# Kernel tuning notes

Measured on AMD Instinct MI355X. Metric: run time of the kernel, lower is better.

The kernel has to match this reference:

```python
import jax, jax.numpy as jnp
import numpy as np

FL = 48  # featurelength


def _sage(x, src, dst, Wl, bl, Wr):
    # PyG SAGEConv (mean aggr): lin_l(mean_{j in N(i)} x_j) + lin_r(x_i); bias on lin_l.
    N = x.shape[0]
    agg = jax.ops.segment_sum(x[src], dst, num_segments=N)
    cnt = jax.ops.segment_sum(jnp.ones((src.shape[0], 1), x.dtype), dst, num_segments=N)
    mean = agg / jnp.maximum(cnt, 1.0)
    return mean @ Wl + bl + x @ Wr


def _pool2(x, H):
    # x: (H*H, C) node features on an HxH grid -> 2x2 max pool -> (H/2*H/2, C)
    C = x.shape[1]
    xc = x.T.reshape(C, H // 2, 2, H // 2, 2)
    return xc.max(axis=(2, 4)).reshape(C, (H // 2) * (H // 2)).T


def _att_block(x, src, dst, am_W, am_b, ax_W, ax_b, c_Wl, c_bl, c_Wr):
    # spatial attention: sigmoid(fc(mean) + fc(max)) over nodes, per-channel gate
    att = jax.nn.sigmoid(jnp.mean(x, 0)[None] @ am_W + am_b + jnp.max(x, 0)[None] @ ax_W + ax_b)
    # channel attention: SAGEConv -> (N,1) gate broadcast over channels
    ch = jax.nn.sigmoid(_sage(x, src, dst, c_Wl, c_bl, c_Wr))
    return x + x * att + x * ch


def setup_inputs() -> dict:
    key = jax.random.key(0)
    ks = iter(jax.random.split(key, 64))
    d = {}
    d['x_image'] = jax.random.normal(next(ks), (128, 128), jnp.float32)
    sizes = [(16384, 65536), (4096, 16384), (1024, 4096), (256, 1024)]
    for i, (n, e) in enumerate(sizes):
        d[f'e{i}'] = jax.random.randint(next(ks), (2, e), 0, n)
    d['train'] = 0

    def lin(kin, kout, k):
        s = 1.0 / np.sqrt(kin)
        return jax.random.uniform(k, (kin, kout), jnp.float32, -s, s)

    # gconv1..4 (in: 1,48,48,48 -> out 48)
    for i, cin in enumerate([1, FL, FL, FL], start=1):
        d[f'g{i}_Wl'] = lin(cin, FL, next(ks))
        d[f'g{i}_bl'] = jnp.zeros((FL,), jnp.float32)
        d[f'g{i}_Wr'] = lin(cin, FL, next(ks))
    # attention blocks 1..4
    for i in range(1, 5):
        d[f'am{i}_W'] = lin(FL, FL, next(ks)); d[f'am{i}_b'] = jnp.zeros((FL,), jnp.float32)
        d[f'ax{i}_W'] = lin(FL, FL, next(ks)); d[f'ax{i}_b'] = jnp.zeros((FL,), jnp.float32)
        d[f'c{i}_Wl'] = lin(FL, 1, next(ks)); d[f'c{i}_bl'] = jnp.zeros((1,), jnp.float32)
        d[f'c{i}_Wr'] = lin(FL, 1, next(ks))
    d['fc1_W'] = lin(FL * 16 * 16, 256, next(ks)); d['fc1_b'] = jnp.zeros((256,), jnp.float32)
    d['fc2_W'] = lin(256, 10, next(ks)); d['fc2_b'] = jnp.zeros((10,), jnp.float32)
    return d


def reference(x_image,
              g1_Wl, g1_bl, g1_Wr, g2_Wl, g2_bl, g2_Wr,
              g3_Wl, g3_bl, g3_Wr, g4_Wl, g4_bl, g4_Wr,
              am1_W, am1_b, ax1_W, ax1_b, c1_Wl, c1_bl, c1_Wr,
              am2_W, am2_b, ax2_W, ax2_b, c2_Wl, c2_bl, c2_Wr,
              am3_W, am3_b, ax3_W, ax3_b, c3_Wl, c3_bl, c3_Wr,
              am4_W, am4_b, ax4_W, ax4_b, c4_Wl, c4_bl, c4_Wr,
              fc1_W, fc1_b, fc2_W, fc2_b,
              e0, e1, e2, e3, train):
    x = x_image.reshape(128 * 128, 1)  # (16384, 1) node features
    # level 1: SAGE on 128x128 graph, pool to 64x64, attention on 64x64 graph (e1)
    x = jax.nn.relu(_sage(x, e0[0], e0[1], g1_Wl, g1_bl, g1_Wr))
    x = _pool2(x, 128)
    x = _att_block(x, e1[0], e1[1], am1_W, am1_b, ax1_W, ax1_b, c1_Wl, c1_bl, c1_Wr)
    # level 2
    x = jax.nn.relu(_sage(x, e1[0], e1[1], g2_Wl, g2_bl, g2_Wr))
    x = _pool2(x, 64)
    x = _att_block(x, e2[0], e2[1], am2_W, am2_b, ax2_W, ax2_b, c2_Wl, c2_bl, c2_Wr)
    # level 3
    x = jax.nn.relu(_sage(x, e2[0], e2[1], g3_Wl, g3_bl, g3_Wr))
    x = _pool2(x, 32)
    x = _att_block(x, e3[0], e3[1], am3_W, am3_b, ax3_W, ax3_b, c3_Wl, c3_bl, c3_Wr)
    # level 4 (no pool; flatten channels-major like torch transpose+reshape)
    x = jax.nn.relu(_sage(x, e3[0], e3[1], g4_Wl, g4_bl, g4_Wr))  # (256, 48)
    x = x.T.reshape(1, FL * 16 * 16)
    x = jax.nn.relu(x @ fc1_W + fc1_b)
    logits = x @ fc2_W + fc2_b
    return jax.nn.log_softmax(logits, axis=1)
```

## Files before the change

### kernel.cpp

```cpp
#include <hip/hip_runtime.h>
#include <math.h>

#define FL 48

__device__ __forceinline__ float sigmoidf(float v) { return 1.0f / (1.0f + expf(-v)); }

__device__ __forceinline__ void att_lds(const float* sum, const float* mxv, float invN,
                                        const float* amW, const float* amb,
                                        const float* axW, const float* axb, float* sAtt) {
  int t = threadIdx.x;
  if (t < FL) {
    float s = amb[t] + axb[t];
    for (int ci = 0; ci < FL; ++ci)
      s += (sum[ci] * invN) * amW[ci * FL + t] + mxv[ci] * axW[ci * FL + t];
    sAtt[t] = sigmoidf(s);
  }
}


__global__ __launch_bounds__(256) void k_prep(
    const int* __restrict__ e0, const int* __restrict__ e1,
    const int* __restrict__ e2, const int* __restrict__ e3,
    const float* __restrict__ ximg,
    float* __restrict__ cnt0, float* __restrict__ cnt1,
    float* __restrict__ cnt2, float* __restrict__ cnt3,
    float* __restrict__ aggS0) {
  int g = blockIdx.x * 256 + threadIdx.x;
  if (g < 65536) {
    int d = e0[65536 + g];
    atomicAdd(&cnt0[d], 1.0f);
    atomicAdd(&aggS0[d], ximg[e0[g]]);
  } else if (g < 81920) {
    atomicAdd(&cnt1[e1[16384 + (g - 65536)]], 1.0f);
  } else if (g < 86016) {
    atomicAdd(&cnt2[e2[4096 + (g - 81920)]], 1.0f);
  } else if (g < 87040) {
    atomicAdd(&cnt3[e3[1024 + (g - 86016)]], 1.0f);
  }
}

__global__ __launch_bounds__(256) void k_scan(
    const float* __restrict__ cnt1, int* __restrict__ off1,
    const float* __restrict__ cnt2, int* __restrict__ off2,
    const float* __restrict__ cnt3, int* __restrict__ off3) {
  const float* cnt; int* off; int N;
  if (blockIdx.x == 0) { cnt = cnt1; off = off1; N = 4096; }
  else if (blockIdx.x == 1) { cnt = cnt2; off = off2; N = 1024; }
  else { cnt = cnt3; off = off3; N = 256; }
  __shared__ int part[256];
  int t = threadIdx.x;
  int chunk = N / 256;
  int base = t * chunk;
  int s = 0;
  for (int i = 0; i < chunk; ++i) s += (int)cnt[base + i];
  part[t] = s;
  __syncthreads();
  for (int o = 1; o < 256; o <<= 1) {
    int v = (t >= o) ? part[t - o] : 0;
    __syncthreads();
    part[t] += v;
    __syncthreads();
  }
  int run = part[t] - s;
  for (int i = 0; i < chunk; ++i) { off[base + i] = run; run += (int)cnt[base + i]; }
  if (t == 255) off[N] = part[255];
}

__global__ __launch_bounds__(256) void k_fill_s1(
    const int* __restrict__ e1, const int* __restrict__ e2, const int* __restrict__ e3,
    const int* __restrict__ off1, int* __restrict__ cur1, int* __restrict__ csr1,
    const int* __restrict__ off2, int* __restrict__ cur2, int* __restrict__ csr2,
    const int* __restrict__ off3, int* __restrict__ cur3, int* __restrict__ csr3,
    const float* __restrict__ ximg, const float* __restrict__ aggS0,
    const float* __restrict__ cnt0,
    const float* __restrict__ Wl, const float* __restrict__ bl, const float* __restrict__ Wr,
    float* __restrict__ xp1) {
  int blk = blockIdx.x;
  if (blk < 84) {
    int i = blk * 256 + threadIdx.x;
    if (i < 16384) {
      int s = e1[i], d = e1[16384 + i];
      csr1[off1[d] + atomicAdd(&cur1[d], 1)] = s;
    } else if (i < 20480) {
      int ii = i - 16384;
      int s = e2[ii], d = e2[4096 + ii];
      csr2[off2[d] + atomicAdd(&cur2[d], 1)] = s;
    } else if (i < 21504) {
      int ii = i - 20480;
      int s = e3[ii], d = e3[1024 + ii];
      csr3[off3[d] + atomicAdd(&cur3[d], 1)] = s;
    }
  } else {
    int g = (blk - 84) * 256 + threadIdx.x;
    if (g < 4096 * FL) {
      int c = g % FL, m = g / FL;
      int a = m >> 6, b = m & 63;
      float wl = Wl[c], wr = Wr[c], bb = bl[c];
      float best = -INFINITY;
#pragma unroll
      for (int da = 0; da < 2; ++da)
#pragma unroll
        for (int db = 0; db < 2; ++db) {
          int n = (2 * a + da) * 128 + (2 * b + db);
          float mean = aggS0[n] / fmaxf(cnt0[n], 1.0f);
          best = fmaxf(best, fmaxf(mean * wl + bb + ximg[n] * wr, 0.0f));
        }
      xp1[g] = best;
    }
  }
}

__global__ __launch_bounds__(256) void k_A(
    const float* __restrict__ x, int N,
    const int* __restrict__ csr, const int* __restrict__ off,
    const float* __restrict__ cntf,
    const float* __restrict__ cWl, const float* __restrict__ cWr,
    const float* __restrict__ cbl,
    float* __restrict__ sum, float* __restrict__ mxv, float* __restrict__ ch) {
  if (blockIdx.x < FL) {
    int c = blockIdx.x, t = threadIdx.x;
    float s = 0.0f, m = -INFINITY;
    for (int n = t; n < N; n += 256) {
      float v = x[n * FL + c];
      s += v; m = fmaxf(m, v);
    }
    __shared__ float ss[256], sm[256];
    ss[t] = s; sm[t] = m;
    __syncthreads();
    for (int o = 128; o > 0; o >>= 1) {
      if (t < o) { ss[t] += ss[t + o]; sm[t] = fmaxf(sm[t], sm[t + o]); }
      __syncthreads();
    }
    if (t == 0) { sum[c] = ss[0]; mxv[c] = sm[0]; }
  } else {
    int n = (blockIdx.x - FL) * 256 + threadIdx.x;
    if (n >= N) return;
    const float* xr = x + n * FL;
    float dr = 0.0f;
    for (int c = 0; c < FL; ++c) dr += xr[c] * cWr[c];
    float g = 0.0f;
    int j0 = off[n], j1 = off[n + 1];
    for (int j = j0; j < j1; ++j) {
      const float* xs = x + csr[j] * FL;
      float a = 0.0f;
      for (int c = 0; c < FL; ++c) a += xs[c] * cWl[c];
      g += a;
    }
    float mean = g / fmaxf(cntf[n], 1.0f);
    ch[n] = sigmoidf(mean + cbl[0] + dr);
  }
}

template <int POOL>
__global__ __launch_bounds__(256) void k_B(
    const float* __restrict__ x, int N, int H,
    const int* __restrict__ csr, const int* __restrict__ off,
    const float* __restrict__ cntf, const float* __restrict__ ch,
    const float* __restrict__ sum, const float* __restrict__ mxv,
    const float* __restrict__ amW, const float* __restrict__ amb,
    const float* __restrict__ axW, const float* __restrict__ axb,
    const float* __restrict__ Wl, const float* __restrict__ bl,
    const float* __restrict__ Wr,
    float* __restrict__ y) {
  const int NS = POOL ? 16 : 4;
  __shared__ float sWl[FL * FL], sWr[FL * FL], sAtt[FL];
  __shared__ float smean[16][FL], sx[16][FL];
  int t = threadIdx.x;
  att_lds(sum, mxv, 1.0f / (float)N, amW, amb, axW, axb, sAtt);
  for (int i = t; i < FL * FL; i += 256) { sWl[i] = Wl[i]; sWr[i] = Wr[i]; }
  __syncthreads();
  int Ho = H >> 1;
  for (int idx = t; idx < NS * FL; idx += 256) {
    int k = idx / FL, ci = idx % FL;
    int m = blockIdx.x * 4 + (POOL ? (k >> 2) : k);
    int n;
    if (POOL) {
      int a = m / Ho, b = m % Ho;
      n = (2 * a + ((k >> 1) & 1)) * H + (2 * b + (k & 1));
    } else {
      n = m;
    }
    float g1 = 1.0f + sAtt[ci];
    float acc = 0.0f;
    for (int j = off[n]; j < off[n + 1]; ++j) {
      int s = csr[j];
      acc += x[s * FL + ci] * (g1 + ch[s]);
    }
    smean[k][ci] = acc / fmaxf(cntf[n], 1.0f);
    sx[k][ci] = x[n * FL + ci] * (g1 + ch[n]);
  }
  __syncthreads();
  if (t < 4 * FL) {
    int q = t / FL, c = t % FL;
    int m = blockIdx.x * 4 + q;
    float best = -INFINITY;
#pragma unroll
    for (int sub = 0; sub < (POOL ? 4 : 1); ++sub) {
      int k = POOL ? q * 4 + sub : q;
      float s = bl[c];
      for (int ci = 0; ci < FL; ++ci)
        s += smean[k][ci] * sWl[ci * FL + c] + sx[k][ci] * sWr[ci * FL + c];
      best = fmaxf(best, fmaxf(s, 0.0f));
    }
    y[m * FL + c] = best;
  }
}

__global__ __launch_bounds__(256) void k_fc1(const float* __restrict__ x4,
                                             const float* __restrict__ W,
                                             float* __restrict__ acc) {
  __shared__ float xin[96];
  int k0 = blockIdx.x * 96;
  int t = threadIdx.x;
  if (t < 96) {
    int k = k0 + t;
    xin[t] = x4[(k & 255) * FL + (k >> 8)];
  }
  __syncthreads();
  float a = 0.0f;
  for (int i = 0; i < 96; ++i) a += xin[i] * W[(size_t)(k0 + i) * 256 + t];
  atomicAdd(&acc[t], a);
}

__global__ void k_final(const float* __restrict__ acc, const float* __restrict__ b1,
                        const float* __restrict__ W2, const float* __restrict__ b2,
                        float* __restrict__ out) {
  __shared__ float av[256];
  __shared__ float logits[10];
  int t = threadIdx.x;
  av[t] = fmaxf(acc[t] + b1[t], 0.0f);
  __syncthreads();
  if (t < 10) {
    float s = b2[t];
    for (int o = 0; o < 256; ++o) s += av[o] * W2[o * 10 + t];
    logits[t] = s;
  }
  __syncthreads();
  if (t == 0) {
    float m = logits[0];
    for (int j = 1; j < 10; ++j) m = fmaxf(m, logits[j]);
    float s = 0.0f;
    for (int j = 0; j < 10; ++j) s += expf(logits[j] - m);
    float ls = logf(s);
    for (int j = 0; j < 10; ++j) out[j] = logits[j] - m - ls;
  }
}


static inline int cdiv(int a, int b) { return (a + b - 1) / b; }

extern "C" void kernel_launch(void* const* d_in, const int* in_sizes, int n_in,
                              void* d_out, int out_size, void* d_ws, size_t ws_size,
                              hipStream_t stream) {
  const float* ximg = (const float*)d_in[0];
  const int* e0 = (const int*)d_in[1];
  const int* e1 = (const int*)d_in[2];
  const int* e2 = (const int*)d_in[3];
  const int* e3 = (const int*)d_in[4];
  const float* g1Wl = (const float*)d_in[6];
  const float* g1bl = (const float*)d_in[7];
  const float* g1Wr = (const float*)d_in[8];
  const float* gWl[3] = {(const float*)d_in[9], (const float*)d_in[12], (const float*)d_in[15]};
  const float* gbl[3] = {(const float*)d_in[10], (const float*)d_in[13], (const float*)d_in[16]};
  const float* gWr[3] = {(const float*)d_in[11], (const float*)d_in[14], (const float*)d_in[17]};
  const float* amW[3]; const float* amb[3]; const float* axW[3]; const float* axb[3];
  const float* cWl[3]; const float* cbl[3]; const float* cWr[3];
  for (int i = 0; i < 3; ++i) {
    int base = 18 + i * 7;
    amW[i] = (const float*)d_in[base + 0];
    amb[i] = (const float*)d_in[base + 1];
    axW[i] = (const float*)d_in[base + 2];
    axb[i] = (const float*)d_in[base + 3];
    cWl[i] = (const float*)d_in[base + 4];
    cbl[i] = (const float*)d_in[base + 5];
    cWr[i] = (const float*)d_in[base + 6];
  }
  const float* fc1W = (const float*)d_in[46];
  const float* fc1b = (const float*)d_in[47];
  const float* fc2W = (const float*)d_in[48];
  const float* fc2b = (const float*)d_in[49];
  float* out = (float*)d_out;

  const int N0 = 16384, N1 = 4096, N2 = 1024, N3 = 256;
  const int E1 = 16384, E2 = 4096, E3 = 1024;

  char* basep = (char*)d_ws;
  size_t off = 0;
  auto alloc = [&](size_t bytes) -> void* {
    void* q = basep + off;
    off += (bytes + 4095) & ~(size_t)4095;
    return q;
  };
  float* cnt0 = (float*)alloc(N0 * 4);
  float* cnt1 = (float*)alloc(N1 * 4);
  float* cnt2 = (float*)alloc(N2 * 4);
  float* cnt3 = (float*)alloc(N3 * 4);
  float* aggS0 = (float*)alloc(N0 * 4);
  int* cur1 = (int*)alloc(N1 * 4);
  int* cur2 = (int*)alloc(N2 * 4);
  int* cur3 = (int*)alloc(N3 * 4);
  float* fc1acc = (float*)alloc(256 * 4);
  size_t zbytes = off;
  int* off1 = (int*)alloc((N1 + 1) * 4);
  int* off2 = (int*)alloc((N2 + 1) * 4);
  int* off3 = (int*)alloc((N3 + 1) * 4);
  int* csr1 = (int*)alloc(E1 * 4);
  int* csr2 = (int*)alloc(E2 * 4);
  int* csr3 = (int*)alloc(E3 * 4);
  float* sum1 = (float*)alloc(FL * 4); float* max1 = (float*)alloc(FL * 4);
  float* sum2 = (float*)alloc(FL * 4); float* max2 = (float*)alloc(FL * 4);
  float* sum3 = (float*)alloc(FL * 4); float* max3 = (float*)alloc(FL * 4);
  float* ch2 = (float*)alloc(N1 * 4);
  float* ch3 = (float*)alloc(N2 * 4);
  float* ch4 = (float*)alloc(N3 * 4);
  float* xp1 = (float*)alloc(N1 * FL * 4);
  float* xp2 = (float*)alloc(N2 * FL * 4);
  float* xp3 = (float*)alloc(N3 * FL * 4);
  float* x4 = (float*)alloc(N3 * FL * 4);

  hipMemsetAsync(d_ws, 0, zbytes, stream);
  k_prep<<<cdiv(87040, 256), 256, 0, stream>>>(e0, e1, e2, e3, ximg,
                                               cnt0, cnt1, cnt2, cnt3, aggS0);
  k_scan<<<3, 256, 0, stream>>>(cnt1, off1, cnt2, off2, cnt3, off3);
  k_fill_s1<<<84 + cdiv(N1 * FL, 256), 256, 0, stream>>>(
      e1, e2, e3, off1, cur1, csr1, off2, cur2, csr2, off3, cur3, csr3,
      ximg, aggS0, cnt0, g1Wl, g1bl, g1Wr, xp1);

  k_A<<<FL + cdiv(N1, 256), 256, 0, stream>>>(xp1, N1, csr1, off1, cnt1,
                                              cWl[0], cWr[0], cbl[0], sum1, max1, ch2);
  k_B<1><<<N2 / 4, 256, 0, stream>>>(xp1, N1, 64, csr1, off1, cnt1, ch2, sum1, max1,
                                     amW[0], amb[0], axW[0], axb[0],
                                     gWl[0], gbl[0], gWr[0], xp2);
  k_A<<<FL + cdiv(N2, 256), 256, 0, stream>>>(xp2, N2, csr2, off2, cnt2,
                                              cWl[1], cWr[1], cbl[1], sum2, max2, ch3);
  k_B<1><<<N3 / 4, 256, 0, stream>>>(xp2, N2, 32, csr2, off2, cnt2, ch3, sum2, max2,
                                     amW[1], amb[1], axW[1], axb[1],
                                     gWl[1], gbl[1], gWr[1], xp3);
  k_A<<<FL + cdiv(N3, 256), 256, 0, stream>>>(xp3, N3, csr3, off3, cnt3,
                                              cWl[2], cWr[2], cbl[2], sum3, max3, ch4);
  k_B<0><<<N3 / 4, 256, 0, stream>>>(xp3, N3, 16, csr3, off3, cnt3, ch4, sum3, max3,
                                     amW[2], amb[2], axW[2], axb[2],
                                     gWl[2], gbl[2], gWr[2], x4);

  k_fc1<<<128, 256, 0, stream>>>(x4, fc1W, fc1acc);
  k_final<<<1, 256, 0, stream>>>(fc1acc, fc1b, fc2W, fc2b, out);

  (void)in_sizes; (void)n_in; (void)out_size; (void)ws_size;
}
```

Baseline: 108.7 us.

## Fuse graph build and attention stats into producer kernels, cut launch count

Builds each CSR (count, scan, fill) inside a single block in shared memory, which replaces the separate prep, scan and fill kernels. The per-node channel-gate dot products and the per-channel sum and max are folded into the epilogue of the producing kernel (k_s1 or k_B), so the k_A launches go away. Consumers rebuild the sigmoid gate from neighbour sums of the dot products. Launches drop from about ten to six, at the cost of redundant neighbour gate computation, atomic float max done through unsigned bit patterns (valid only while values are non-negative, as after ReLU), and padded accumulators to spread atomic contention.

Result: slower. 156.0 us (+43.6%).

```diff
diff --git a/kernel.cpp b/kernel.cpp
--- a/kernel.cpp
+++ b/kernel.cpp
@@ -2,57 +2,50 @@
 #include <math.h>
 
 #define FL 48
+#define STP 16
 
 __device__ __forceinline__ float sigmoidf(float v) { return 1.0f / (1.0f + expf(-v)); }
 
-__device__ __forceinline__ void att_lds(const float* sum, const float* mxv, float invN,
-                                        const float* amW, const float* amb,
-                                        const float* axW, const float* axb, float* sAtt) {
-  int t = threadIdx.x;
-  if (t < FL) {
-    float s = amb[t] + axb[t];
-    for (int ci = 0; ci < FL; ++ci)
-      s += (sum[ci] * invN) * amW[ci * FL + t] + mxv[ci] * axW[ci * FL + t];
-    sAtt[t] = sigmoidf(s);
-  }
-}
-
-
-__global__ __launch_bounds__(256) void k_prep(
-    const int* __restrict__ e0, const int* __restrict__ e1,
-    const int* __restrict__ e2, const int* __restrict__ e3,
-    const float* __restrict__ ximg,
-    float* __restrict__ cnt0, float* __restrict__ cnt1,
-    float* __restrict__ cnt2, float* __restrict__ cnt3,
-    float* __restrict__ aggS0) {
-  int g = blockIdx.x * 256 + threadIdx.x;
-  if (g < 65536) {
-    int d = e0[65536 + g];
+__device__ __forceinline__ float ch_node(int s, const int* __restrict__ csr,
+                                         const int* __restrict__ off,
+                                         const float* __restrict__ dl,
+                                         const float* __restrict__ dr, float cb) {
+  int j0 = off[s], j1 = off[s + 1];
+  float g = 0.0f;
+  for (int j = j0; j < j1; ++j) g += dl[csr[j]];
+  return sigmoidf(g / fmaxf((float)(j1 - j0), 1.0f) + cb + dr[s]);
+}
+
+
+__global__ __launch_bounds__(256) void k_graph(
+    const int* __restrict__ e0, const float* __restrict__ ximg,
+    float* __restrict__ cnt0, float* __restrict__ aggS0,
+    const int* __restrict__ e1, int* __restrict__ off1, int* __restrict__ csr1,
+    const int* __restrict__ e2, int* __restrict__ off2, int* __restrict__ csr2,
+    const int* __restrict__ e3, int* __restrict__ off3, int* __restrict__ csr3) {
+  int blk = blockIdx.x;
+  if (blk < 256) {
+    int i = blk * 256 + threadIdx.x;
+    int d = e0[65536 + i];
     atomicAdd(&cnt0[d], 1.0f);
-    atomicAdd(&aggS0[d], ximg[e0[g]]);
-  } else if (g < 81920) {
-    atomicAdd(&cnt1[e1[16384 + (g - 65536)]], 1.0f);
-  } else if (g < 86016) {
-    atomicAdd(&cnt2[e2[4096 + (g - 81920)]], 1.0f);
-  } else if (g < 87040) {
-    atomicAdd(&cnt3[e3[1024 + (g - 86016)]], 1.0f);
-  }
-}
-
-__global__ __launch_bounds__(256) void k_scan(
-    const float* __restrict__ cnt1, int* __restrict__ off1,
-    const float* __restrict__ cnt2, int* __restrict__ off2,
-    const float* __restrict__ cnt3, int* __restrict__ off3) {
-  const float* cnt; int* off; int N;
-  if (blockIdx.x == 0) { cnt = cnt1; off = off1; N = 4096; }
-  else if (blockIdx.x == 1) { cnt = cnt2; off = off2; N = 1024; }
-  else { cnt = cnt3; off = off3; N = 256; }
+    atomicAdd(&aggS0[d], ximg[e0[i]]);
+    return;
+  }
+  __shared__ int buf[4096];
   __shared__ int part[256];
-  int t = threadIdx.x;
+  const int* e; int* off; int* csr; int N, E;
+  if (blk == 256)      { e = e1; off = off1; csr = csr1; N = 4096; E = 16384; }
+  else if (blk == 257) { e = e2; off = off2; csr = csr2; N = 1024; E = 4096; }
+  else                 { e = e3; off = off3; csr = csr3; N = 256;  E = 1024; }
+  int t = threadIdx.x;
+  for (int n = t; n < N; n += 256) buf[n] = 0;
+  __syncthreads();
+  for (int i = t; i < E; i += 256) atomicAdd(&buf[e[E + i]], 1);
+  __syncthreads();
   int chunk = N / 256;
   int base = t * chunk;
   int s = 0;
-  for (int i = 0; i < chunk; ++i) s += (int)cnt[base + i];
+  for (int i = 0; i < chunk; ++i) s += buf[base + i];
   part[t] = s;
   __syncthreads();
   for (int o = 1; o < 256; o <<= 1) {
@@ -62,134 +55,139 @@
     __syncthreads();
   }
   int run = part[t] - s;
-  for (int i = 0; i < chunk; ++i) { off[base + i] = run; run += (int)cnt[base + i]; }
-  if (t == 255) off[N] = part[255];
-}
-
-__global__ __launch_bounds__(256) void k_fill_s1(
-    const int* __restrict__ e1, const int* __restrict__ e2, const int* __restrict__ e3,
-    const int* __restrict__ off1, int* __restrict__ cur1, int* __restrict__ csr1,
-    const int* __restrict__ off2, int* __restrict__ cur2, int* __restrict__ csr2,
-    const int* __restrict__ off3, int* __restrict__ cur3, int* __restrict__ csr3,
+  for (int i = 0; i < chunk; ++i) {
+    int c = buf[base + i];
+    off[base + i] = run;
+    buf[base + i] = run;
+    run += c;
+  }
+  if (t == 255) off[N] = E;
+  __syncthreads();
+  for (int i = t; i < E; i += 256) {
+    int d = e[E + i];
+    int pos = atomicAdd(&buf[d], 1);
+    csr[pos] = e[i];
+  }
+}
+
+__global__ __launch_bounds__(256) void k_s1(
     const float* __restrict__ ximg, const float* __restrict__ aggS0,
     const float* __restrict__ cnt0,
-    const float* __restrict__ Wl, const float* __restrict__ bl, const float* __restrict__ Wr,
-    float* __restrict__ xp1) {
-  int blk = blockIdx.x;
-  if (blk < 84) {
-    int i = blk * 256 + threadIdx.x;
-    if (i < 16384) {
-      int s = e1[i], d = e1[16384 + i];
-      csr1[off1[d] + atomicAdd(&cur1[d], 1)] = s;
-    } else if (i < 20480) {
-      int ii = i - 16384;
-      int s = e2[ii], d = e2[4096 + ii];
-      csr2[off2[d] + atomicAdd(&cur2[d], 1)] = s;
-    } else if (i < 21504) {
-      int ii = i - 20480;
-      int s = e3[ii], d = e3[1024 + ii];
-      csr3[off3[d] + atomicAdd(&cur3[d], 1)] = s;
-    }
-  } else {
-    int g = (blk - 84) * 256 + threadIdx.x;
-    if (g < 4096 * FL) {
-      int c = g % FL, m = g / FL;
-      int a = m >> 6, b = m & 63;
-      float wl = Wl[c], wr = Wr[c], bb = bl[c];
-      float best = -INFINITY;
+    const float* __restrict__ Wl, const float* __restrict__ bl,
+    const float* __restrict__ Wr,
+    const float* __restrict__ cWl, const float* __restrict__ cWr,
+    float* __restrict__ y, float* __restrict__ dl, float* __restrict__ dr,
+    float* __restrict__ sumP, float* __restrict__ maxP) {
+  __shared__ float ldl[4], ldr[4], lsum[FL];
+  __shared__ unsigned lmax[FL];
+  int t = threadIdx.x;
+  if (t < 4) { ldl[t] = 0.0f; ldr[t] = 0.0f; }
+  if (t < FL) { lsum[t] = 0.0f; lmax[t] = 0u; }
+  __syncthreads();
+  if (t < 4 * FL) {
+    int q = t / FL, c = t % FL;
+    int m = blockIdx.x * 4 + q;
+    int a = m >> 6, b = m & 63;
+    float wl = Wl[c], wr = Wr[c], bb = bl[c];
+    float best = -INFINITY;
 #pragma unroll
-      for (int da = 0; da < 2; ++da)
+    for (int da = 0; da < 2; ++da)
 #pragma unroll
-        for (int db = 0; db < 2; ++db) {
-          int n = (2 * a + da) * 128 + (2 * b + db);
-          float mean = aggS0[n] / fmaxf(cnt0[n], 1.0f);
-          best = fmaxf(best, fmaxf(mean * wl + bb + ximg[n] * wr, 0.0f));
-        }
-      xp1[g] = best;
-    }
-  }
-}
-
-__global__ __launch_bounds__(256) void k_A(
-    const float* __restrict__ x, int N,
-    const int* __restrict__ csr, const int* __restrict__ off,
-    const float* __restrict__ cntf,
-    const float* __restrict__ cWl, const float* __restrict__ cWr,
-    const float* __restrict__ cbl,
-    float* __restrict__ sum, float* __restrict__ mxv, float* __restrict__ ch) {
-  if (blockIdx.x < FL) {
-    int c = blockIdx.x, t = threadIdx.x;
-    float s = 0.0f, m = -INFINITY;
-    for (int n = t; n < N; n += 256) {
-      float v = x[n * FL + c];
-      s += v; m = fmaxf(m, v);
-    }
-    __shared__ float ss[256], sm[256];
-    ss[t] = s; sm[t] = m;
-    __syncthreads();
-    for (int o = 128; o > 0; o >>= 1) {
-      if (t < o) { ss[t] += ss[t + o]; sm[t] = fmaxf(sm[t], sm[t + o]); }
-      __syncthreads();
-    }
-    if (t == 0) { sum[c] = ss[0]; mxv[c] = sm[0]; }
-  } else {
-    int n = (blockIdx.x - FL) * 256 + threadIdx.x;
-    if (n >= N) return;
-    const float* xr = x + n * FL;
-    float dr = 0.0f;
-    for (int c = 0; c < FL; ++c) dr += xr[c] * cWr[c];
-    float g = 0.0f;
-    int j0 = off[n], j1 = off[n + 1];
-    for (int j = j0; j < j1; ++j) {
-      const float* xs = x + csr[j] * FL;
-      float a = 0.0f;
-      for (int c = 0; c < FL; ++c) a += xs[c] * cWl[c];
-      g += a;
-    }
-    float mean = g / fmaxf(cntf[n], 1.0f);
-    ch[n] = sigmoidf(mean + cbl[0] + dr);
-  }
-}
-
-template <int POOL>
+      for (int db = 0; db < 2; ++db) {
+        int n = (2 * a + da) * 128 + (2 * b + db);
+        float mean = aggS0[n] / fmaxf(cnt0[n], 1.0f);
+        best = fmaxf(best, fmaxf(mean * wl + bb + ximg[n] * wr, 0.0f));
+      }
+    y[m * FL + c] = best;
+    atomicAdd(&ldl[q], best * cWl[c]);
+    atomicAdd(&ldr[q], best * cWr[c]);
+    atomicAdd(&lsum[c], best);
+    atomicMax(&lmax[c], __float_as_uint(best));
+  }
+  __syncthreads();
+  if (t < 4) { int m = blockIdx.x * 4 + t; dl[m] = ldl[t]; dr[m] = ldr[t]; }
+  if (t < FL) {
+    atomicAdd(&sumP[t * STP], lsum[t]);
+    atomicMax((unsigned*)&maxP[t * STP], lmax[t]);
+  }
+}
+
+template <int POOL, int HAS_NEXT>
 __global__ __launch_bounds__(256) void k_B(
     const float* __restrict__ x, int N, int H,
     const int* __restrict__ csr, const int* __restrict__ off,
-    const float* __restrict__ cntf, const float* __restrict__ ch,
-    const float* __restrict__ sum, const float* __restrict__ mxv,
+    const float* __restrict__ dl, const float* __restrict__ dr,
+    const float* __restrict__ cbl,
+    const float* __restrict__ sumP, const float* __restrict__ maxP,
     const float* __restrict__ amW, const float* __restrict__ amb,
     const float* __restrict__ axW, const float* __restrict__ axb,
     const float* __restrict__ Wl, const float* __restrict__ bl,
     const float* __restrict__ Wr,
-    float* __restrict__ y) {
+    float* __restrict__ y,
+    float* __restrict__ ndl, float* __restrict__ ndr,
+    const float* __restrict__ ncWl, const float* __restrict__ ncWr,
+    float* __restrict__ nsum, float* __restrict__ nmax) {
   const int NS = POOL ? 16 : 4;
   __shared__ float sWl[FL * FL], sWr[FL * FL], sAtt[FL];
   __shared__ float smean[16][FL], sx[16][FL];
-  int t = threadIdx.x;
-  att_lds(sum, mxv, 1.0f / (float)N, amW, amb, axW, axb, sAtt);
+  __shared__ float chE[16][32], chS[16], rcS[16];
+  __shared__ float ldl[4], ldr[4], lsum[FL];
+  __shared__ unsigned lmax[FL];
+  int t = threadIdx.x;
+  int Ho = H >> 1;
+  float cb = cbl[0];
+
+  auto node_of = [&](int k) -> int {
+    int m = blockIdx.x * 4 + (POOL ? (k >> 2) : k);
+    if (POOL) {
+      int a = m / Ho, b = m % Ho;
+      return (2 * a + ((k >> 1) & 1)) * H + (2 * b + (k & 1));
+    }
+    return m;
+  };
+
+  if (t < FL) {
+    float s = amb[t] + axb[t];
+    float invN = 1.0f / (float)N;
+    for (int ci = 0; ci < FL; ++ci)
+      s += (sumP[ci * STP] * invN) * amW[ci * FL + t] + maxP[ci * STP] * axW[ci * FL + t];
+    sAtt[t] = sigmoidf(s);
+  }
   for (int i = t; i < FL * FL; i += 256) { sWl[i] = Wl[i]; sWr[i] = Wr[i]; }
-  __syncthreads();
-  int Ho = H >> 1;
+  if (HAS_NEXT) {
+    if (t < 4) { ldl[t] = 0.0f; ldr[t] = 0.0f; }
+    if (t < FL) { lsum[t] = 0.0f; lmax[t] = 0u; }
+  }
+  if (t < NS) {
+    int n = node_of(t);
+    chS[t] = ch_node(n, csr, off, dl, dr, cb);
+    rcS[t] = 1.0f / fmaxf((float)(off[n + 1] - off[n]), 1.0f);
+  }
+  for (int idx = t; idx < NS * 32; idx += 256) {
+    int k = idx >> 5, r = idx & 31;
+    int n = node_of(k);
+    int j = off[n] + r;
+    if (j < off[n + 1]) chE[k][r] = ch_node(csr[j], csr, off, dl, dr, cb);
+  }
+  __syncthreads();
+
   for (int idx = t; idx < NS * FL; idx += 256) {
     int k = idx / FL, ci = idx % FL;
-    int m = blockIdx.x * 4 + (POOL ? (k >> 2) : k);
-    int n;
-    if (POOL) {
-      int a = m / Ho, b = m % Ho;
-      n = (2 * a + ((k >> 1) & 1)) * H + (2 * b + (k & 1));
-    } else {
-      n = m;
-    }
+    int n = node_of(k);
+    int j0 = off[n], j1 = off[n + 1];
     float g1 = 1.0f + sAtt[ci];
     float acc = 0.0f;
-    for (int j = off[n]; j < off[n + 1]; ++j) {
+    for (int j = j0; j < j1; ++j) {
       int s = csr[j];
-      acc += x[s * FL + ci] * (g1 + ch[s]);
-    }
-    smean[k][ci] = acc / fmaxf(cntf[n], 1.0f);
-    sx[k][ci] = x[n * FL + ci] * (g1 + ch[n]);
-  }
-  __syncthreads();
+      int r = j - j0;
+      float chv = (r < 32) ? chE[k][r] : ch_node(s, csr, off, dl, dr, cb);
+      acc += x[s * FL + ci] * (g1 + chv);
+    }
+    smean[k][ci] = acc * rcS[k];
+    sx[k][ci] = x[n * FL + ci] * (g1 + chS[k]);
+  }
+  __syncthreads();
+
   if (t < 4 * FL) {
     int q = t / FL, c = t % FL;
     int m = blockIdx.x * 4 + q;
@@ -203,12 +201,26 @@
       best = fmaxf(best, fmaxf(s, 0.0f));
     }
     y[m * FL + c] = best;
+    if (HAS_NEXT) {
+      atomicAdd(&ldl[q], best * ncWl[c]);
+      atomicAdd(&ldr[q], best * ncWr[c]);
+      atomicAdd(&lsum[c], best);
+      atomicMax(&lmax[c], __float_as_uint(best));
+    }
+  }
+  if (HAS_NEXT) {
+    __syncthreads();
+    if (t < 4) { int m = blockIdx.x * 4 + t; ndl[m] = ldl[t]; ndr[m] = ldr[t]; }
+    if (t < FL) {
+      atomicAdd(&nsum[t * STP], lsum[t]);
+      atomicMax((unsigned*)&nmax[t * STP], lmax[t]);
+    }
   }
 }
 
 __global__ __launch_bounds__(256) void k_fc1(const float* __restrict__ x4,
                                              const float* __restrict__ W,
-                                             float* __restrict__ acc) {
+                                             float* __restrict__ accP) {
   __shared__ float xin[96];
   int k0 = blockIdx.x * 96;
   int t = threadIdx.x;
@@ -219,16 +231,16 @@
   __syncthreads();
   float a = 0.0f;
   for (int i = 0; i < 96; ++i) a += xin[i] * W[(size_t)(k0 + i) * 256 + t];
-  atomicAdd(&acc[t], a);
-}
-
-__global__ void k_final(const float* __restrict__ acc, const float* __restrict__ b1,
+  atomicAdd(&accP[t * STP], a);
+}
+
+__global__ void k_final(const float* __restrict__ accP, const float* __restrict__ b1,
                         const float* __restrict__ W2, const float* __restrict__ b2,
                         float* __restrict__ out) {
   __shared__ float av[256];
   __shared__ float logits[10];
   int t = threadIdx.x;
-  av[t] = fmaxf(acc[t] + b1[t], 0.0f);
+  av[t] = fmaxf(accP[t * STP] + b1[t], 0.0f);
   __syncthreads();
   if (t < 10) {
     float s = b2[t];
@@ -292,14 +304,11 @@
     return q;
   };
   float* cnt0 = (float*)alloc(N0 * 4);
-  float* cnt1 = (float*)alloc(N1 * 4);
-  float* cnt2 = (float*)alloc(N2 * 4);
-  float* cnt3 = (float*)alloc(N3 * 4);
   float* aggS0 = (float*)alloc(N0 * 4);
-  int* cur1 = (int*)alloc(N1 * 4);
-  int* cur2 = (int*)alloc(N2 * 4);
-  int* cur3 = (int*)alloc(N3 * 4);
-  float* fc1acc = (float*)alloc(256 * 4);
+  float* fc1acc = (float*)alloc(256 * STP * 4);
+  float* sum1 = (float*)alloc(FL * STP * 4); float* max1 = (float*)alloc(FL * STP * 4);
+  float* sum2 = (float*)alloc(FL * STP * 4); float* max2 = (float*)alloc(FL * STP * 4);
+  float* sum3 = (float*)alloc(FL * STP * 4); float* max3 = (float*)alloc(FL * STP * 4);
   size_t zbytes = off;
   int* off1 = (int*)alloc((N1 + 1) * 4);
   int* off2 = (int*)alloc((N2 + 1) * 4);
@@ -307,41 +316,33 @@
   int* csr1 = (int*)alloc(E1 * 4);
   int* csr2 = (int*)alloc(E2 * 4);
   int* csr3 = (int*)alloc(E3 * 4);
-  float* sum1 = (float*)alloc(FL * 4); float* max1 = (float*)alloc(FL * 4);
-  float* sum2 = (float*)alloc(FL * 4); float* max2 = (float*)alloc(FL * 4);
-  float* sum3 = (float*)alloc(FL * 4); float* max3 = (float*)alloc(FL * 4);
-  float* ch2 = (float*)alloc(N1 * 4);
-  float* ch3 = (float*)alloc(N2 * 4);
-  float* ch4 = (float*)alloc(N3 * 4);
+  float* dl2 = (float*)alloc(N1 * 4); float* dr2 = (float*)alloc(N1 * 4);
+  float* dl3 = (float*)alloc(N2 * 4); float* dr3 = (float*)alloc(N2 * 4);
+  float* dl4 = (float*)alloc(N3 * 4); float* dr4 = (float*)alloc(N3 * 4);
   float* xp1 = (float*)alloc(N1 * FL * 4);
   float* xp2 = (float*)alloc(N2 * FL * 4);
   float* xp3 = (float*)alloc(N3 * FL * 4);
   float* x4 = (float*)alloc(N3 * FL * 4);
 
   hipMemsetAsync(d_ws, 0, zbytes, stream);
-  k_prep<<<cdiv(87040, 256), 256, 0, stream>>>(e0, e1, e2, e3, ximg,
-                                               cnt0, cnt1, cnt2, cnt3, aggS0);
-  k_scan<<<3, 256, 0, stream>>>(cnt1, off1, cnt2, off2, cnt3, off3);
-  k_fill_s1<<<84 + cdiv(N1 * FL, 256), 256, 0, stream>>>(
-      e1, e2, e3, off1, cur1, csr1, off2, cur2, csr2, off3, cur3, csr3,
-      ximg, aggS0, cnt0, g1Wl, g1bl, g1Wr, xp1);
-
-  k_A<<<FL + cdiv(N1, 256), 256, 0, stream>>>(xp1, N1, csr1, off1, cnt1,
-                                              cWl[0], cWr[0], cbl[0], sum1, max1, ch2);
-  k_B<1><<<N2 / 4, 256, 0, stream>>>(xp1, N1, 64, csr1, off1, cnt1, ch2, sum1, max1,
-                                     amW[0], amb[0], axW[0], axb[0],
-                                     gWl[0], gbl[0], gWr[0], xp2);
-  k_A<<<FL + cdiv(N2, 256), 256, 0, stream>>>(xp2, N2, csr2, off2, cnt2,
-                                              cWl[1], cWr[1], cbl[1], sum2, max2, ch3);
-  k_B<1><<<N3 / 4, 256, 0, stream>>>(xp2, N2, 32, csr2, off2, cnt2, ch3, sum2, max2,
-                                     amW[1], amb[1], axW[1], axb[1],
-                                     gWl[1], gbl[1], gWr[1], xp3);
-  k_A<<<FL + cdiv(N3, 256), 256, 0, stream>>>(xp3, N3, csr3, off3, cnt3,
-                                              cWl[2], cWr[2], cbl[2], sum3, max3, ch4);
-  k_B<0><<<N3 / 4, 256, 0, stream>>>(xp3, N3, 16, csr3, off3, cnt3, ch4, sum3, max3,
-                                     amW[2], amb[2], axW[2], axb[2],
-                                     gWl[2], gbl[2], gWr[2], x4);
-
+  k_graph<<<259, 256, 0, stream>>>(e0, ximg, cnt0, aggS0,
+                                   e1, off1, csr1, e2, off2, csr2, e3, off3, csr3);
+  k_s1<<<N1 / 4, 256, 0, stream>>>(ximg, aggS0, cnt0, g1Wl, g1bl, g1Wr,
+                                   cWl[0], cWr[0], xp1, dl2, dr2, sum1, max1);
+  k_B<1, 1><<<N2 / 4, 256, 0, stream>>>(xp1, N1, 64, csr1, off1, dl2, dr2, cbl[0],
+                                        sum1, max1, amW[0], amb[0], axW[0], axb[0],
+                                        gWl[0], gbl[0], gWr[0], xp2,
+                                        dl3, dr3, cWl[1], cWr[1], sum2, max2);
+  k_B<1, 1><<<N3 / 4, 256, 0, stream>>>(xp2, N2, 32, csr2, off2, dl3, dr3, cbl[1],
+                                        sum2, max2, amW[1], amb[1], axW[1], axb[1],
+                                        gWl[1], gbl[1], gWr[1], xp3,
+                                        dl4, dr4, cWl[2], cWr[2], sum3, max3);
+  k_B<0, 0><<<N3 / 4, 256, 0, stream>>>(xp3, N3, 16, csr3, off3, dl4, dr4, cbl[2],
+                                        sum3, max3, amW[2], amb[2], axW[2], axb[2],
+                                        gWl[2], gbl[2], gWr[2], x4,
+                                        (float*)nullptr, (float*)nullptr,
+                                        (const float*)nullptr, (const float*)nullptr,
+                                        (float*)nullptr, (float*)nullptr);
   k_fc1<<<128, 256, 0, stream>>>(x4, fc1W, fc1acc);
   k_final<<<1, 256, 0, stream>>>(fc1acc, fc1b, fc2W, fc2b, out);
 
```
